# Performance work log

Measured on AMD Instinct MI355X. Metric: run time of the kernel, lower is better.

Reference implementation:

```python
import jax, jax.numpy as jnp
import numpy as np

BATCH = 64
ALPHA = 1.0
BETA = 1.0
THRESH_DEG = 2.0
# deg2dist: chordal distance on the unit sphere for an angle in degrees
THRESH = 2.0 * np.sin(np.deg2rad(THRESH_DEG) / 2.0)
THRESH2 = np.float32(THRESH * THRESH)


def score_mean_var(A):
    """Per-observation mean/variance of exp(-0.5*A*z2) for z2 ~ U[0,4] truncated at THRESH2.
    (z2 = |u_pred - u_obs|^2 is uniform on [0,4] for u_obs uniform on the unit sphere.)"""
    half = 0.5 * A * THRESH2
    mu = (1.0 - jnp.exp(-half)) / (2.0 * A)          # E[score]
    e2 = (1.0 - jnp.exp(-2.0 * half)) / (4.0 * A)    # E[score^2]
    return mu, e2 - mu * mu


def setup_inputs() -> dict:
    key = jax.random.key(0)
    k1, k2 = jax.random.split(key)
    # scale 0.02 so a realistic fraction of z2 lands below THRESH2 (~1.2e-3)
    z = jax.random.normal(k1, (BATCH, 1000, 128, 3), dtype=jnp.float32) * 0.02
    R = jax.random.uniform(k2, (BATCH, 1), dtype=jnp.float32, minval=0.01, maxval=0.1)
    num_obs = jnp.float32(85000.0)
    return {"z": z, "R": R, "num_obs": num_obs}


def reference(z, R, num_obs):
    A = 1.0 / (R * R)                         # (B, 1)
    Bc = (-0.5 * A).reshape(BATCH, 1, 1)      # (B, 1, 1)
    z2 = jnp.sum(z * z, axis=-1)              # (B, T, O)
    # fused: square-sum -> threshold -> exp -> mask -> reduce (no scatter_nd needed)
    raw_scores = jnp.where(z2 < THRESH2, jnp.exp(Bc * z2), jnp.float32(0.0))
    raw_score = jnp.sum(raw_scores, axis=(1, 2))  # (B,)
    mu_per_obs, sigma2_per_obs = score_mean_var(A[:, 0])
    mu = num_obs * mu_per_obs
    sigma2 = num_obs * sigma2_per_obs
    objective = raw_score - ALPHA * mu - BETA * sigma2
    return raw_score, mu, sigma2, objective
```

## Files before the change

### kernel.cpp

```cpp
#include <hip/hip_runtime.h>
#include <math.h>

#define BATCH 64
#define TOBS (1000 * 128)
#define GROUPS (TOBS / 4)
#define BPB 25
#define BLOCK 256

__global__ __launch_bounds__(BLOCK) void score_kernel(const float* __restrict__ z,
                                                      const float* __restrict__ R,
                                                      float* __restrict__ ws,
                                                      float thresh2) {
    const int b = blockIdx.x / BPB;
    const int chunk = blockIdx.x % BPB;
    const float r = R[b];
    const float Bc = -0.5f / (r * r);
    const float4* __restrict__ zb = (const float4*)(z + (size_t)b * (TOBS * 3));

    float acc = 0.0f;
    const int g0 = chunk * BLOCK + threadIdx.x;
    #pragma unroll
    for (int i = 0; i < 5; ++i) {
        const int g = g0 + i * (BPB * BLOCK);
        const float4 a0 = zb[g * 3 + 0];
        const float4 a1 = zb[g * 3 + 1];
        const float4 a2 = zb[g * 3 + 2];
        const float z20 = a0.x * a0.x + a0.y * a0.y + a0.z * a0.z;
        const float z21 = a0.w * a0.w + a1.x * a1.x + a1.y * a1.y;
        const float z22 = a1.z * a1.z + a1.w * a1.w + a2.x * a2.x;
        const float z23 = a2.y * a2.y + a2.z * a2.z + a2.w * a2.w;
        acc += (z20 < thresh2) ? __expf(Bc * z20) : 0.0f;
        acc += (z21 < thresh2) ? __expf(Bc * z21) : 0.0f;
        acc += (z22 < thresh2) ? __expf(Bc * z22) : 0.0f;
        acc += (z23 < thresh2) ? __expf(Bc * z23) : 0.0f;
    }

    #pragma unroll
    for (int off = 32; off > 0; off >>= 1)
        acc += __shfl_down(acc, off, 64);

    __shared__ float wave_sums[BLOCK / 64];
    const int wave = threadIdx.x >> 6;
    const int lane = threadIdx.x & 63;
    if (lane == 0) wave_sums[wave] = acc;
    __syncthreads();
    if (threadIdx.x == 0) {
        float t = 0.0f;
        #pragma unroll
        for (int w = 0; w < BLOCK / 64; ++w) t += wave_sums[w];
        ws[blockIdx.x] = t;
    }
}

__global__ void finalize_kernel(const float* __restrict__ ws,
                                const float* __restrict__ R,
                                const float* __restrict__ num_obs,
                                float* __restrict__ out,
                                float thresh2) {
    const int b = threadIdx.x;
    if (b >= BATCH) return;

    float rs = 0.0f;
    #pragma unroll
    for (int c = 0; c < BPB; ++c) rs += ws[b * BPB + c];

    const float r = R[b];
    const float A = 1.0f / (r * r);
    const float half = 0.5f * A * thresh2;
    const float mu_p = (1.0f - expf(-half)) / (2.0f * A);
    const float e2 = (1.0f - expf(-2.0f * half)) / (4.0f * A);
    const float var = e2 - mu_p * mu_p;
    const float nobs = num_obs[0];
    const float mu = nobs * mu_p;
    const float s2 = nobs * var;
    out[b] = rs;
    out[BATCH + b] = mu;
    out[2 * BATCH + b] = s2;
    out[3 * BATCH + b] = rs - mu - s2;
}

extern "C" void kernel_launch(void* const* d_in, const int* in_sizes, int n_in,
                              void* d_out, int out_size, void* d_ws, size_t ws_size,
                              hipStream_t stream) {
    const float* z = (const float*)d_in[0];
    const float* R = (const float*)d_in[1];
    const float* num_obs = (const float*)d_in[2];
    float* out = (float*)d_out;
    float* ws = (float*)d_ws;

    const double th = 2.0 * sin(M_PI / 180.0);
    const float thresh2 = (float)(th * th);

    score_kernel<<<dim3(BATCH * BPB), dim3(BLOCK), 0, stream>>>(z, R, ws, thresh2);
    finalize_kernel<<<dim3(1), dim3(64), 0, stream>>>(ws, R, num_obs, out, thresh2);
}
```

Before: 146.3 us.

## Stage z through LDS with async global_load_lds and double buffering

Replaces the strided per-thread float4 loads with async global-to-LDS loads (global_load_lds, 16 bytes per lane). Each wave gets its own double-buffered LDS slot, and the next iteration is prefetched while the current one computes. Lane addresses are permuted and reads swizzled so the global loads stay coalesced and the LDS reads avoid bank conflicts. This adds manual vmcnt waits and per-wave LDS use, and relies on the permutation math being exactly right.

```diff
diff --git a/kernel.cpp b/kernel.cpp
--- a/kernel.cpp
+++ b/kernel.cpp
@@ -6,25 +6,64 @@
 #define GROUPS (TOBS / 4)
 #define BPB 25
 #define BLOCK 256
+#define ITERS 5
+
+__device__ __forceinline__ void gload_lds16(const float4* g, float4* l) {
+    __builtin_amdgcn_global_load_lds(
+        (const __attribute__((address_space(1))) void*)g,
+        (__attribute__((address_space(3))) void*)l,
+        16, 0, 0);
+}
 
 __global__ __launch_bounds__(BLOCK) void score_kernel(const float* __restrict__ z,
                                                       const float* __restrict__ R,
                                                       float* __restrict__ ws,
                                                       float thresh2) {
+    __shared__ float4 stage[8][192];
+
     const int b = blockIdx.x / BPB;
     const int chunk = blockIdx.x % BPB;
+    const int w = threadIdx.x >> 6;
+    const int l = threadIdx.x & 63;
+
     const float r = R[b];
     const float Bc = -0.5f / (r * r);
+    asm volatile("s_waitcnt vmcnt(0)" ::: "memory");
+
     const float4* __restrict__ zb = (const float4*)(z + (size_t)b * (TOBS * 3));
 
+    const int lperm = (61 * l) & 63;
+    const int f0 = 3 * l, f1 = 3 * l + 1, f2 = 3 * l + 2;
+    const int rd0 = (f0 & 192) + ((21 * (f0 & 63)) & 63);
+    const int rd1 = (f1 & 192) + ((21 * (f1 & 63)) & 63);
+    const int rd2 = (f2 & 192) + ((21 * (f2 & 63)) & 63);
+
+    const int base_grp = chunk * BLOCK + w * 64;
+
+    {
+        const float4* s = zb + (size_t)3 * base_grp + lperm;
+        gload_lds16(s,       &stage[w * 2 + 0][0]);
+        gload_lds16(s + 64,  &stage[w * 2 + 0][64]);
+        gload_lds16(s + 128, &stage[w * 2 + 0][128]);
+    }
+
     float acc = 0.0f;
-    const int g0 = chunk * BLOCK + threadIdx.x;
     #pragma unroll
-    for (int i = 0; i < 5; ++i) {
-        const int g = g0 + i * (BPB * BLOCK);
-        const float4 a0 = zb[g * 3 + 0];
-        const float4 a1 = zb[g * 3 + 1];
-        const float4 a2 = zb[g * 3 + 2];
+    for (int i = 0; i < ITERS; ++i) {
+        const int p = i & 1;
+        if (i + 1 < ITERS) {
+            const float4* s = zb + (size_t)3 * (base_grp + (i + 1) * (BPB * BLOCK)) + lperm;
+            gload_lds16(s,       &stage[w * 2 + (p ^ 1)][0]);
+            gload_lds16(s + 64,  &stage[w * 2 + (p ^ 1)][64]);
+            gload_lds16(s + 128, &stage[w * 2 + (p ^ 1)][128]);
+            asm volatile("s_waitcnt vmcnt(3)" ::: "memory");
+        } else {
+            asm volatile("s_waitcnt vmcnt(0)" ::: "memory");
+        }
+
+        const float4 a0 = stage[w * 2 + p][rd0];
+        const float4 a1 = stage[w * 2 + p][rd1];
+        const float4 a2 = stage[w * 2 + p][rd2];
         const float z20 = a0.x * a0.x + a0.y * a0.y + a0.z * a0.z;
         const float z21 = a0.w * a0.w + a1.x * a1.x + a1.y * a1.y;
         const float z22 = a1.z * a1.z + a1.w * a1.w + a2.x * a2.x;
@@ -47,7 +86,7 @@
     if (threadIdx.x == 0) {
         float t = 0.0f;
         #pragma unroll
-        for (int w = 0; w < BLOCK / 64; ++w) t += wave_sums[w];
+        for (int ww = 0; ww < BLOCK / 64; ++ww) t += wave_sums[ww];
         ws[blockIdx.x] = t;
     }
 }
```

Result: no change. 145.8 us (-0.3%).
